# Optimization experiments

Hardware: AMD Instinct MI355X
Metric: run time of the kernel (lower is better)

## Reference

```python
import jax, jax.numpy as jnp
import numpy as np

# dims: L=seq_len, B=batch, D=n_d (hidden), PROJ=n_proj, H=heads, DEPTH=layers, V=vocab
L, B, D, PROJ, H, DEPTH, V = 1024, 4, 1024, 256, 8, 4, 32000
HD = PROJ // H          # head dim = 32
NEG = -10000.0          # additive causal mask value used by Model.set_mask


def setup_inputs() -> dict:
    key = jax.random.key(0)
    ks = jax.random.split(key, 12)
    s = (3.0 / D) ** 0.5  # init used by Model.init_weights (layer_norm-style)
    return {
        "x": jax.random.randint(ks[0], (L, B), 0, V),
        "y": jax.random.randint(ks[1], (L, B), 0, V),
        "hidden": jnp.zeros((DEPTH, B, D), jnp.float32),            # init_hidden
        "emb_W": jax.random.uniform(ks[2], (V, D), jnp.float32, -s, s),
        # SRU++ attention transform per layer: q-proj, kv-proj, output to 3*D (U matrices)
        "W1": jax.random.normal(ks[3], (DEPTH, D, PROJ), jnp.float32) / np.float32(np.sqrt(D)),
        "W2": jax.random.normal(ks[4], (DEPTH, PROJ, 2 * PROJ), jnp.float32) / np.float32(np.sqrt(PROJ)),
        "W3": jax.random.normal(ks[5], (DEPTH, PROJ, 3 * D), jnp.float32) / np.float32(np.sqrt(PROJ)),
        "alpha": jax.random.normal(ks[6], (DEPTH,), jnp.float32) * 0.1,  # rezero scalar (nonzero so attn path is live)
        "weight_c": jax.random.normal(ks[7], (DEPTH, 2 * D), jnp.float32) * 0.1,  # (v_f, v_r)
        # bias = (b_f, b_r); forget bias initialized to highway_bias = -3
        "bias": jnp.concatenate([jnp.full((DEPTH, D), -3.0, jnp.float32), jnp.zeros((DEPTH, D), jnp.float32)], axis=-1),
        "Wout": jax.random.uniform(ks[8], (D, V), jnp.float32, -s, s),
        "bout": jnp.zeros((V,), jnp.float32),
    }


def _attention_transform(h, W1, W2, W3, alpha, mask):
    # SRUppAttention (no memory, no layer_norm, dropout=0)
    z = jnp.einsum('lbd,dp->lbp', h, W1)                 # (L,B,PROJ) query / residual
    kv = jnp.einsum('lbp,pq->lbq', z, W2)                # (L,B,2*PROJ)
    k, v = jnp.split(kv, 2, axis=-1)
    q = z.reshape(L, B, H, HD) * (HD ** -0.5)
    k = k.reshape(L, B, H, HD)
    v = v.reshape(L, B, H, HD)
    scores = jnp.einsum('lbhd,sbhd->bhls', q, k) + mask  # causal additive mask
    attn = jax.nn.softmax(scores, axis=-1)
    out = jnp.einsum('bhls,sbhd->lbhd', attn, v).reshape(L, B, PROJ)
    out = out * alpha + z                                # rezero residual
    return jnp.einsum('lbp,pk->lbk', out, W3)            # U: (L,B,3*D)


def _sru_recurrence(U, residual, c0, vf, vr, bf, br):
    # SRU elementwise highway recurrence (k=3, identity activation, no rescale)
    u = U.reshape(L, B, D, 3)
    u0 = u[..., 0]
    u1 = u[..., 1] + bf
    u2 = u[..., 2] + br

    def step(c, xs):
        u0t, u1t, u2t, rt = xs                           # each (B,D)
        f = jax.nn.sigmoid(u1t + vf * c)
        c = f * c + (1.0 - f) * u0t
        r = jax.nn.sigmoid(u2t + vr * c)
        h = r * c + (1.0 - r) * rt                       # highway on layer input
        return c, h

    c_last, hs = jax.lax.scan(step, c0, (u0, u1, u2, residual))
    return hs, c_last


def reference(x, y, hidden, emb_W, W1, W2, W3, alpha, weight_c, bias, Wout, bout):
    mask = jnp.triu(jnp.full((L, L), NEG, jnp.float32), 1)   # Model.set_mask, mem_len=0
    h = emb_W[x]                                             # (L,B,D) embedding lookup
    for i in range(DEPTH):
        U = _attention_transform(h, W1[i], W2[i], W3[i], alpha[i], mask)
        h, _ = _sru_recurrence(U, h, hidden[i],
                               weight_c[i, :D], weight_c[i, D:],
                               bias[i, :D], bias[i, D:])
    logits = jnp.einsum('lbd,dv->lbv', h, Wout) + bout       # (L,B,V)
    logp = jax.nn.log_softmax(logits, axis=-1)
    loss = -jnp.take_along_axis(logp, y[..., None], axis=-1)[..., 0]  # (L,B) per-token CE
    return loss
```

## Files before the change

### kernel.cpp

```cpp
#include <hip/hip_runtime.h>
#include <hip/hip_bf16.h>
#include <stdint.h>

#define L_ 1024
#define B_ 4
#define D_ 1024
#define PROJ_ 256
#define H_ 8
#define V_ 32000
#define M_ 4096

typedef __bf16 bf16x8 __attribute__((ext_vector_type(8)));
typedef float f32x4 __attribute__((ext_vector_type(4)));

#define AS3(p) ((__attribute__((address_space(3))) void*)(p))
#define AS1(p) ((const __attribute__((address_space(1))) void*)(p))

__global__ __launch_bounds__(256) void k_embed(const int* __restrict__ x,
                                               const float* __restrict__ emb,
                                               __hip_bfloat16* __restrict__ h) {
  int gid = blockIdx.x * 256 + threadIdx.x;
  int row = gid >> 8;
  int d0 = (gid & 255) << 2;
  int tok = x[row];
  const float4 v = *(const float4*)(emb + (size_t)tok * D_ + d0);
  union { __hip_bfloat16 o[4]; uint2 u; } cv;
  cv.o[0] = __float2bfloat16(v.x);
  cv.o[1] = __float2bfloat16(v.y);
  cv.o[2] = __float2bfloat16(v.z);
  cv.o[3] = __float2bfloat16(v.w);
  *(uint2*)(h + (size_t)row * D_ + d0) = cv.u;
}

__global__ __launch_bounds__(256) void k_transpose(const float* __restrict__ in,
                                                   __hip_bfloat16* __restrict__ out,
                                                   int K, int N,
                                                   long in_stride, long out_stride) {
  __shared__ float t[64][65];
  in += (size_t)blockIdx.z * in_stride;
  out += (size_t)blockIdx.z * out_stride;
  int n0 = blockIdx.x * 64, k0 = blockIdx.y * 64;
  int r = threadIdx.x >> 4, c4 = (threadIdx.x & 15) << 2;
#pragma unroll
  for (int p = 0; p < 4; p++) {
    float4 v = *(const float4*)(in + (size_t)(k0 + p * 16 + r) * N + n0 + c4);
    t[p * 16 + r][c4 + 0] = v.x;
    t[p * 16 + r][c4 + 1] = v.y;
    t[p * 16 + r][c4 + 2] = v.z;
    t[p * 16 + r][c4 + 3] = v.w;
  }
  __syncthreads();
  int n = threadIdx.x >> 2, kg = (threadIdx.x & 3) << 4;
  union { __hip_bfloat16 b[16]; uint4 u[2]; } cv;
#pragma unroll
  for (int i = 0; i < 16; i++) cv.b[i] = __float2bfloat16(t[kg + i][n]);
  uint4* op = (uint4*)(out + (size_t)(n0 + n) * K + k0 + kg);
  op[0] = cv.u[0];
  op[1] = cv.u[1];
}

template <bool CLS>
__global__ __launch_bounds__(256) void k_gemm_bt(
    const __hip_bfloat16* __restrict__ A, const __hip_bfloat16* __restrict__ Bt,
    __hip_bfloat16* __restrict__ C, int K, int N,
    const float* __restrict__ bout, const int* __restrict__ y,
    float2* __restrict__ lse, float* __restrict__ logitY) {
  __shared__ __hip_bfloat16 As[128 * 64];
  __shared__ __hip_bfloat16 Bs[128 * 64];
  const int tid = threadIdx.x;
  const int lane = tid & 63, wave = tid >> 6;
  const int quad = lane >> 4, l16 = lane & 15;
  const int wm = wave & 1, wn = wave >> 1;
  const int row0 = blockIdx.x * 128, col0 = blockIdx.y * 128;

  f32x4 acc[4][4] = {};

  const __hip_bfloat16* Abase = A + (size_t)row0 * K;
  const __hip_bfloat16* Bbase = Bt + (size_t)col0 * K;
  const int m_s = tid >> 3;
  const int ko_sw = (((tid & 7) ^ (m_s & 7)) << 3);
  const int xr = l16 & 7;

  for (int k0 = 0; k0 < K; k0 += 64) {
    __syncthreads();
#pragma unroll
    for (int call = 0; call < 4; call++) {
      int m = m_s + call * 32;
      __builtin_amdgcn_global_load_lds(AS1(Abase + (size_t)m * K + k0 + ko_sw),
                                       AS3(As + (call * 256 + wave * 64) * 8),
                                       16, 0, 0);
      __builtin_amdgcn_global_load_lds(AS1(Bbase + (size_t)m * K + k0 + ko_sw),
                                       AS3(Bs + (call * 256 + wave * 64) * 8),
                                       16, 0, 0);
    }
    __syncthreads();
#pragma unroll
    for (int kk = 0; kk < 2; kk++) {
      bf16x8 af[4], bfr[4];
#pragma unroll
      for (int mi = 0; mi < 4; mi++)
        af[mi] = *(const bf16x8*)(As + (wm * 64 + mi * 16 + l16) * 64 +
                                  (((kk * 4 + quad) ^ xr) << 3));
#pragma unroll
      for (int ni = 0; ni < 4; ni++)
        bfr[ni] = *(const bf16x8*)(Bs + (wn * 64 + ni * 16 + l16) * 64 +
                                   (((kk * 4 + quad) ^ xr) << 3));
#pragma unroll
      for (int mi = 0; mi < 4; mi++)
#pragma unroll
        for (int ni = 0; ni < 4; ni++)
          acc[mi][ni] = __builtin_amdgcn_mfma_f32_16x16x32_bf16(af[mi], bfr[ni],
                                                                acc[mi][ni], 0, 0, 0);
    }
  }

  if constexpr (!CLS) {
#pragma unroll
    for (int mi = 0; mi < 4; mi++)
#pragma unroll
      for (int ni = 0; ni < 4; ni++)
#pragma unroll
        for (int r = 0; r < 4; r++) {
          int row = row0 + wm * 64 + mi * 16 + quad * 4 + r;
          int col = col0 + wn * 64 + ni * 16 + l16;
          C[(size_t)row * N + col] = __float2bfloat16(acc[mi][ni][r]);
        }
  } else {
    const int chunk = blockIdx.y * 2 + wn;
    float bv[4];
#pragma unroll
    for (int ni = 0; ni < 4; ni++)
      bv[ni] = bout[col0 + wn * 64 + ni * 16 + l16];
#pragma unroll
    for (int mi = 0; mi < 4; mi++) {
#pragma unroll
      for (int r = 0; r < 4; r++) {
        int row = row0 + wm * 64 + mi * 16 + quad * 4 + r;
        float v0 = acc[mi][0][r] + bv[0];
        float v1 = acc[mi][1][r] + bv[1];
        float v2 = acc[mi][2][r] + bv[2];
        float v3 = acc[mi][3][r] + bv[3];
        int yv = y[row];
        int cb = col0 + wn * 64 + l16;
        if (yv == cb + 0)  logitY[row] = v0;
        if (yv == cb + 16) logitY[row] = v1;
        if (yv == cb + 32) logitY[row] = v2;
        if (yv == cb + 48) logitY[row] = v3;
        float m = fmaxf(fmaxf(v0, v1), fmaxf(v2, v3));
#pragma unroll
        for (int off = 1; off < 16; off <<= 1)
          m = fmaxf(m, __shfl_xor(m, off, 64));
        float s = __expf(v0 - m) + __expf(v1 - m) + __expf(v2 - m) + __expf(v3 - m);
#pragma unroll
        for (int off = 1; off < 16; off <<= 1)
          s += __shfl_xor(s, off, 64);
        if (l16 == 0)
          lse[(size_t)chunk * M_ + row] = make_float2(m, s);
      }
    }
  }
}

__global__ __launch_bounds__(512, 2) void k_gemm_cls256(
    const __hip_bfloat16* __restrict__ A, const __hip_bfloat16* __restrict__ Bt,
    int K, const float* __restrict__ bout, const int* __restrict__ y,
    float2* __restrict__ lse, float* __restrict__ logitY) {
  __shared__ __align__(16) __hip_bfloat16 As[2][16384];
  __shared__ __align__(16) __hip_bfloat16 Bs[2][16384];
  const int tid = threadIdx.x;
  const int lane = tid & 63, wave = tid >> 6;
  const int quad = lane >> 4, l16 = lane & 15;
  const int wm = wave >> 2, wn = wave & 3;

  const int bid = blockIdx.y * 16 + blockIdx.x;
  const int swzb = (bid & 7) * 250 + (bid >> 3);
  const int bx = swzb & 15, by = swzb >> 4;
  const int row0 = bx * 256, col0 = by * 256;

  const int m_l = wave * 8 + (lane >> 3);
  const int sw = ((lane & 7) ^ (lane >> 3)) << 3;
  const __hip_bfloat16* Ag = A + (size_t)(row0 + m_l) * K + sw;
  const __hip_bfloat16* Bg = Bt + (size_t)(col0 + m_l) * K + sw;

#define STAGE_A(buf, r, ko)                                                   \
  __builtin_amdgcn_global_load_lds(AS1(Ag + (size_t)(r) * 64 * K + (ko)),     \
                                   AS3(&As[buf][((r) * 64 + wave * 8) * 64]), \
                                   16, 0, 0)
#define STAGE_B(buf, r, ko)                                                   \
  __builtin_amdgcn_global_load_lds(AS1(Bg + (size_t)(r) * 64 * K + (ko)),     \
                                   AS3(&Bs[buf][((r) * 64 + wave * 8) * 64]), \
                                   16, 0, 0)

  const int aoff = (wm * 128 + l16) * 64;
  const int boff = (wn * 64 + l16) * 64;
  const int cc0 = ((quad) ^ (l16 & 7)) << 3;
  const int cc1 = ((4 + quad) ^ (l16 & 7)) << 3;

  f32x4 acc[8][4] = {};
  bf16x8 a4[4], b0[4], b1[4];

#define DS_B(buf, breg, cck)                                                  \
  do {                                                                        \
    _Pragma("unroll") for (int ni = 0; ni < 4; ++ni)                          \
        breg[ni] = *(const bf16x8*)(&Bs[buf][boff + ni * 1024 + (cck)]);      \
  } while (0)

#define DS_A(buf, mlo, cck)                                                   \
  do {                                                                        \
    _Pragma("unroll") for (int mi = 0; mi < 4; ++mi)                          \
        a4[mi] = *(const bf16x8*)(&As[buf][aoff + ((mlo) + mi) * 1024 + (cck)]); \
  } while (0)

#define MFMA_Q(mlo, breg)                                                     \
  do {                                                                        \
    __builtin_amdgcn_s_barrier();                                             \
    asm volatile("s_waitcnt lgkmcnt(0)" ::: "memory");                        \
    __builtin_amdgcn_sched_barrier(0);                                        \
    __builtin_amdgcn_s_setprio(1);                                            \
    _Pragma("unroll") for (int mi = 0; mi < 4; ++mi)                          \
        _Pragma("unroll") for (int ni = 0; ni < 4; ++ni)                      \
            acc[(mlo) + mi][ni] = __builtin_amdgcn_mfma_f32_16x16x32_bf16(    \
                a4[mi], breg[ni], acc[(mlo) + mi][ni], 0, 0, 0);              \
    __builtin_amdgcn_s_setprio(0);                                            \
  } while (0)

#define BAR() __builtin_amdgcn_s_barrier()

  STAGE_A(0, 0, 0); STAGE_A(0, 1, 0); STAGE_A(0, 2, 0); STAGE_A(0, 3, 0);
  STAGE_B(0, 0, 0); STAGE_B(0, 1, 0); STAGE_B(0, 2, 0); STAGE_B(0, 3, 0);
  STAGE_B(1, 0, 64); STAGE_B(1, 1, 64); STAGE_B(1, 2, 64); STAGE_B(1, 3, 64);
  asm volatile("s_waitcnt vmcnt(4)" ::: "memory");
  BAR();

  for (int i = 0; i < 7; ++i) {
    const size_t kT1 = (size_t)i * 128 + 64;
    const size_t kN0 = (size_t)i * 128 + 128;
    const size_t kN1 = (size_t)i * 128 + 192;
    DS_B(0, b0, cc0); DS_A(0, 0, cc0);
    STAGE_A(1, 0, kT1); STAGE_A(1, 1, kT1); STAGE_A(1, 2, kT1); STAGE_A(1, 3, kT1);
    MFMA_Q(0, b0); BAR();
    DS_B(0, b1, cc1); DS_A(0, 0, cc1);
    MFMA_Q(0, b1); BAR();
    DS_A(0, 4, cc0);
    STAGE_B(0, 0, kN0); STAGE_B(0, 1, kN0);
    MFMA_Q(4, b0); BAR();
    DS_A(0, 4, cc1);
    STAGE_B(0, 2, kN0); STAGE_B(0, 3, kN0);
    MFMA_Q(4, b1);
    asm volatile("s_waitcnt vmcnt(4)" ::: "memory");
    BAR();
    DS_B(1, b0, cc0); DS_A(1, 0, cc0);
    STAGE_A(0, 0, kN0); STAGE_A(0, 1, kN0); STAGE_A(0, 2, kN0); STAGE_A(0, 3, kN0);
    MFMA_Q(0, b0); BAR();
    DS_B(1, b1, cc1); DS_A(1, 0, cc1);
    MFMA_Q(0, b1); BAR();
    DS_A(1, 4, cc0);
    STAGE_B(1, 0, kN1); STAGE_B(1, 1, kN1);
    MFMA_Q(4, b0); BAR();
    DS_A(1, 4, cc1);
    STAGE_B(1, 2, kN1); STAGE_B(1, 3, kN1);
    MFMA_Q(4, b1);
    asm volatile("s_waitcnt vmcnt(4)" ::: "memory");
    BAR();
  }
  {
    const size_t kT1 = (size_t)7 * 128 + 64;
    DS_B(0, b0, cc0); DS_A(0, 0, cc0);
    STAGE_A(1, 0, kT1); STAGE_A(1, 1, kT1); STAGE_A(1, 2, kT1); STAGE_A(1, 3, kT1);
    MFMA_Q(0, b0); BAR();
    DS_B(0, b1, cc1); DS_A(0, 0, cc1);
    MFMA_Q(0, b1); BAR();
    DS_A(0, 4, cc0);
    MFMA_Q(4, b0); BAR();
    DS_A(0, 4, cc1);
    MFMA_Q(4, b1);
    asm volatile("s_waitcnt vmcnt(0)" ::: "memory");
    BAR();
    DS_B(1, b0, cc0); DS_A(1, 0, cc0);
    MFMA_Q(0, b0); BAR();
    DS_B(1, b1, cc1); DS_A(1, 0, cc1);
    MFMA_Q(0, b1); BAR();
    DS_A(1, 4, cc0);
    MFMA_Q(4, b0); BAR();
    DS_A(1, 4, cc1);
    MFMA_Q(4, b1);
  }

  const int chunk = by * 4 + wn;
  float bv[4];
#pragma unroll
  for (int ni = 0; ni < 4; ++ni)
    bv[ni] = bout[col0 + wn * 64 + ni * 16 + l16];
#pragma unroll
  for (int mi = 0; mi < 8; ++mi) {
#pragma unroll
    for (int r = 0; r < 4; ++r) {
      int row = row0 + wm * 128 + mi * 16 + quad * 4 + r;
      float v0 = acc[mi][0][r] + bv[0];
      float v1 = acc[mi][1][r] + bv[1];
      float v2 = acc[mi][2][r] + bv[2];
      float v3 = acc[mi][3][r] + bv[3];
      int yv = y[row];
      int cb = col0 + wn * 64 + l16;
      if (yv == cb + 0)  logitY[row] = v0;
      if (yv == cb + 16) logitY[row] = v1;
      if (yv == cb + 32) logitY[row] = v2;
      if (yv == cb + 48) logitY[row] = v3;
      float m = fmaxf(fmaxf(v0, v1), fmaxf(v2, v3));
#pragma unroll
      for (int off = 1; off < 16; off <<= 1)
        m = fmaxf(m, __shfl_xor(m, off, 64));
      float s = __expf(v0 - m) + __expf(v1 - m) + __expf(v2 - m) + __expf(v3 - m);
#pragma unroll
      for (int off = 1; off < 16; off <<= 1)
        s += __shfl_xor(s, off, 64);
      if (l16 == 0)
        lse[(size_t)chunk * M_ + row] = make_float2(m, s);
    }
  }
#undef STAGE_A
#undef STAGE_B
#undef DS_A
#undef DS_B
#undef MFMA_Q
#undef BAR
}

__global__ __launch_bounds__(256) void k_gemm_cls_f32(
    const __hip_bfloat16* __restrict__ A, const float* __restrict__ B,
    int K, int N, const float* __restrict__ bout, const int* __restrict__ y,
    float2* __restrict__ lse, float* __restrict__ logitY) {
  __shared__ __hip_bfloat16 As[128 * 40];
  __shared__ __hip_bfloat16 Bs[128 * 40];
  const int tid = threadIdx.x;
  const int lane = tid & 63, wave = tid >> 6;
  const int quad = lane >> 4, l16 = lane & 15;
  const int wm = wave & 1, wn = wave >> 1;
  const int row0 = blockIdx.x * 128, col0 = blockIdx.y * 128;
  f32x4 acc[4][4] = {};
  const int a_m = tid >> 1, a_k = (tid & 1) << 4;
  const int b_k = tid >> 3, b_n = (tid & 7) << 4;
  for (int k0 = 0; k0 < K; k0 += 32) {
    const uint4* ap = (const uint4*)(A + (size_t)(row0 + a_m) * K + k0 + a_k);
    uint4 av0 = ap[0];
    uint4 av1 = ap[1];
    const float* bp = B + (size_t)(k0 + b_k) * N + col0 + b_n;
    float4 bv0 = *(const float4*)(bp + 0);
    float4 bv1 = *(const float4*)(bp + 4);
    float4 bv2 = *(const float4*)(bp + 8);
    float4 bv3 = *(const float4*)(bp + 12);
    __syncthreads();
    *(uint4*)(As + a_m * 40 + a_k) = av0;
    *(uint4*)(As + a_m * 40 + a_k + 8) = av1;
    {
      float tmp[16] = {bv0.x, bv0.y, bv0.z, bv0.w, bv1.x, bv1.y, bv1.z, bv1.w,
                       bv2.x, bv2.y, bv2.z, bv2.w, bv3.x, bv3.y, bv3.z, bv3.w};
#pragma unroll
      for (int j = 0; j < 16; j++)
        Bs[(b_n + j) * 40 + b_k] = __float2bfloat16(tmp[j]);
    }
    __syncthreads();
    bf16x8 af[4], bfr[4];
#pragma unroll
    for (int mi = 0; mi < 4; mi++)
      af[mi] = *(const bf16x8*)(As + (wm * 64 + mi * 16 + l16) * 40 + quad * 8);
#pragma unroll
    for (int ni = 0; ni < 4; ni++)
      bfr[ni] = *(const bf16x8*)(Bs + (wn * 64 + ni * 16 + l16) * 40 + quad * 8);
#pragma unroll
    for (int mi = 0; mi < 4; mi++)
#pragma unroll
      for (int ni = 0; ni < 4; ni++)
        acc[mi][ni] = __builtin_amdgcn_mfma_f32_16x16x32_bf16(af[mi], bfr[ni],
                                                              acc[mi][ni], 0, 0, 0);
  }
  const int chunk = blockIdx.y * 2 + wn;
  float bv[4];
#pragma unroll
  for (int ni = 0; ni < 4; ni++)
    bv[ni] = bout[col0 + wn * 64 + ni * 16 + l16];
#pragma unroll
  for (int mi = 0; mi < 4; mi++) {
#pragma unroll
    for (int r = 0; r < 4; r++) {
      int row = row0 + wm * 64 + mi * 16 + quad * 4 + r;
      float v0 = acc[mi][0][r] + bv[0];
      float v1 = acc[mi][1][r] + bv[1];
      float v2 = acc[mi][2][r] + bv[2];
      float v3 = acc[mi][3][r] + bv[3];
      int yv = y[row];
      int cb = col0 + wn * 64 + l16;
      if (yv == cb + 0)  logitY[row] = v0;
      if (yv == cb + 16) logitY[row] = v1;
      if (yv == cb + 32) logitY[row] = v2;
      if (yv == cb + 48) logitY[row] = v3;
      float m = fmaxf(fmaxf(v0, v1), fmaxf(v2, v3));
#pragma unroll
      for (int off = 1; off < 16; off <<= 1)
        m = fmaxf(m, __shfl_xor(m, off, 64));
      float s = __expf(v0 - m) + __expf(v1 - m) + __expf(v2 - m) + __expf(v3 - m);
#pragma unroll
      for (int off = 1; off < 16; off <<= 1)
        s += __shfl_xor(s, off, 64);
      if (l16 == 0)
        lse[(size_t)chunk * M_ + row] = make_float2(m, s);
    }
  }
}

__global__ __launch_bounds__(256) void k_attn_mfma(
    const __hip_bfloat16* __restrict__ z, const __hip_bfloat16* __restrict__ kv,
    __hip_bfloat16* __restrict__ ao, const float* __restrict__ alpha_p) {
  __shared__ __hip_bfloat16 Qs[64 * 40];
  __shared__ __hip_bfloat16 Ks[128 * 40];
  __shared__ __hip_bfloat16 Vt[32 * 136];
  __shared__ __hip_bfloat16 Ps[64 * 136];
  const int tid = threadIdx.x;
  const int lane = tid & 63, wave = tid >> 6;
  const int quad = lane >> 4, l16 = lane & 15;
  const int bh = blockIdx.y, b = bh >> 3, h = bh & 7;
  const int q0 = blockIdx.x * 64;
  const float scale = 0.17677669529663687f;

  {
    int r = tid >> 2, c = (tid & 3) << 3;
    *(uint4*)(Qs + r * 40 + c) =
        *(const uint4*)(z + ((size_t)(q0 + r) * B_ + b) * PROJ_ + h * 32 + c);
  }

  float m_i[4] = {-1e30f, -1e30f, -1e30f, -1e30f};
  float l_i[4] = {0.f, 0.f, 0.f, 0.f};
  f32x4 o_acc[2] = {};

  const int ntile = (q0 + 191) >> 7;

  for (int t = 0; t < ntile; t++) {
    const int s0 = t << 7;
    __syncthreads();
    {
      int r = tid >> 1, c = (tid & 1) << 4;
      const uint4* kp =
          (const uint4*)(kv + ((size_t)(s0 + r) * B_ + b) * 512 + h * 32 + c);
      *(uint4*)(Ks + r * 40 + c) = kp[0];
      *(uint4*)(Ks + r * 40 + c + 8) = kp[1];
    }
    {
      int s = tid >> 1, dbase = (tid & 1) << 4;
      const __hip_bfloat16* vp =
          kv + ((size_t)(s0 + s) * B_ + b) * 512 + 256 + h * 32 + dbase;
      union { uint4 u; __hip_bfloat16 e[8]; } t0, t1;
      t0.u = *(const uint4*)vp;
      t1.u = *(const uint4*)(vp + 8);
#pragma unroll
      for (int j = 0; j < 8; j++) {
        Vt[(dbase + j) * 136 + s] = t0.e[j];
        Vt[(dbase + 8 + j) * 136 + s] = t1.e[j];
      }
    }
    __syncthreads();

    f32x4 sacc[8] = {};
    {
      bf16x8 aq = *(const bf16x8*)(Qs + (wave * 16 + l16) * 40 + quad * 8);
#pragma unroll
      for (int ni = 0; ni < 8; ni++) {
        bf16x8 bk = *(const bf16x8*)(Ks + (ni * 16 + l16) * 40 + quad * 8);
        sacc[ni] = __builtin_amdgcn_mfma_f32_16x16x32_bf16(aq, bk, sacc[ni], 0, 0, 0);
      }
    }

#pragma unroll
    for (int r = 0; r < 4; r++) {
      const int qrow = q0 + wave * 16 + quad * 4 + r;
      float mx = -1e30f;
#pragma unroll
      for (int ni = 0; ni < 8; ni++) {
        int s = s0 + ni * 16 + l16;
        float v = (s <= qrow) ? sacc[ni][r] * scale : -1e30f;
        sacc[ni][r] = v;
        mx = fmaxf(mx, v);
      }
#pragma unroll
      for (int off = 1; off < 16; off <<= 1)
        mx = fmaxf(mx, __shfl_xor(mx, off, 64));
      float mnew = fmaxf(m_i[r], mx);
      float al = __expf(m_i[r] - mnew);
      m_i[r] = mnew;
      float ps = 0.f;
#pragma unroll
      for (int ni = 0; ni < 8; ni++) {
        float p = __expf(sacc[ni][r] - mnew);
        Ps[(wave * 16 + quad * 4 + r) * 136 + ni * 16 + l16] = __float2bfloat16(p);
        ps += p;
      }
#pragma unroll
      for (int off = 1; off < 16; off <<= 1)
        ps += __shfl_xor(ps, off, 64);
      l_i[r] = l_i[r] * al + ps;
      o_acc[0][r] *= al;
      o_acc[1][r] *= al;
    }

#pragma unroll
    for (int ks = 0; ks < 4; ks++) {
      bf16x8 ap = *(const bf16x8*)(Ps + (wave * 16 + l16) * 136 + ks * 32 + quad * 8);
#pragma unroll
      for (int ni = 0; ni < 2; ni++) {
        bf16x8 bv = *(const bf16x8*)(Vt + (ni * 16 + l16) * 136 + ks * 32 + quad * 8);
        o_acc[ni] = __builtin_amdgcn_mfma_f32_16x16x32_bf16(ap, bv, o_acc[ni], 0, 0, 0);
      }
    }
  }

  const float arz = alpha_p[0];
#pragma unroll
  for (int ni = 0; ni < 2; ni++)
#pragma unroll
    for (int r = 0; r < 4; r++) {
      int row = q0 + wave * 16 + quad * 4 + r;
      size_t oi = ((size_t)row * B_ + b) * PROJ_ + h * 32 + ni * 16 + l16;
      float res = __bfloat162float(z[oi]);
      ao[oi] = __float2bfloat16(o_acc[ni][r] / l_i[r] * arz + res);
    }
}

__global__ __launch_bounds__(64) void k_sru(const __hip_bfloat16* __restrict__ U,
                                            __hip_bfloat16* __restrict__ h,
                                            const float* __restrict__ hidden,
                                            const float* __restrict__ wc,
                                            const float* __restrict__ bias) {
  int tid = blockIdx.x * 64 + threadIdx.x;
  int b = tid >> 10, d = tid & 1023;
  float vf = wc[d], vr = wc[D_ + d];
  float bfs = bias[d], brs = bias[D_ + d];
  float c = hidden[b * D_ + d];
  const __hip_bfloat16* up = U + (size_t)b * 3 * D_ + 3 * d;
  __hip_bfloat16* hp = h + (size_t)b * D_ + d;
  const int US = B_ * 3 * D_, HS = B_ * D_;
  for (int l0 = 0; l0 < L_; l0 += 8) {
    float u0[8], u1[8], u2[8], rs[8];
#pragma unroll
    for (int j = 0; j < 8; j++) {
      u0[j] = __bfloat162float(up[(size_t)j * US + 0]);
      u1[j] = __bfloat162float(up[(size_t)j * US + 1]);
      u2[j] = __bfloat162float(up[(size_t)j * US + 2]);
      rs[j] = __bfloat162float(hp[(size_t)j * HS]);
    }
#pragma unroll
    for (int j = 0; j < 8; j++) {
      float f = __builtin_amdgcn_rcpf(1.f + __expf(-(u1[j] + bfs + vf * c)));
      c = u0[j] + f * (c - u0[j]);
      float r = __builtin_amdgcn_rcpf(1.f + __expf(-(u2[j] + brs + vr * c)));
      hp[(size_t)j * HS] = __float2bfloat16(rs[j] + r * (c - rs[j]));
    }
    up += (size_t)8 * US;
    hp += (size_t)8 * HS;
  }
}

__global__ __launch_bounds__(256) void k_finalize(const float2* __restrict__ lse,
                                                  const float* __restrict__ logitY,
                                                  float* __restrict__ out) {
  int row = blockIdx.x * 256 + threadIdx.x;
  float M = -1e30f, S = 0.f;
  for (int c = 0; c < V_ / 64; c++) {
    float2 p = lse[(size_t)c * M_ + row];
    if (p.x > M) {
      S = S * __expf(M - p.x) + p.y;
      M = p.x;
    } else {
      S += p.y * __expf(p.x - M);
    }
  }
  out[row] = M + logf(S) - logitY[row];
}

extern "C" void kernel_launch(void* const* d_in, const int* in_sizes, int n_in,
                              void* d_out, int out_size, void* d_ws, size_t ws_size,
                              hipStream_t stream) {
  const int* x = (const int*)d_in[0];
  const int* y = (const int*)d_in[1];
  const float* hidden = (const float*)d_in[2];
  const float* emb = (const float*)d_in[3];
  const float* W1 = (const float*)d_in[4];
  const float* W2 = (const float*)d_in[5];
  const float* W3 = (const float*)d_in[6];
  const float* alpha = (const float*)d_in[7];
  const float* wc = (const float*)d_in[8];
  const float* bias = (const float*)d_in[9];
  const float* Wout = (const float*)d_in[10];
  const float* bout = (const float*)d_in[11];

  char* ws = (char*)d_ws;
  __hip_bfloat16* h16  = (__hip_bfloat16*)(ws + 0);
  __hip_bfloat16* z16  = (__hip_bfloat16*)(ws + 8388608);
  __hip_bfloat16* kv16 = (__hip_bfloat16*)(ws + 10485760);
  __hip_bfloat16* ao16 = (__hip_bfloat16*)(ws + 14680064);
  __hip_bfloat16* W1t  = (__hip_bfloat16*)(ws + 16777216);
  __hip_bfloat16* W2t  = (__hip_bfloat16*)(ws + 18874368);
  __hip_bfloat16* W3t  = (__hip_bfloat16*)(ws + 19922944);
  __hip_bfloat16* U16  = (__hip_bfloat16*)(ws + 26214400);
  const bool fast = ws_size >= 109723648ull;
  __hip_bfloat16* Woutt = (__hip_bfloat16*)(ws + 26214400);
  float2* lse    = (float2*)(ws + (fast ? 93323264u : 26214400u));
  float* logitY  = (float*)(ws + (fast ? 109707264u : 42598400u));
  float* out     = (float*)d_out;

  k_embed<<<4096, 256, 0, stream>>>(x, emb, h16);
  k_transpose<<<dim3(4, 16, 4), 256, 0, stream>>>(W1, W1t, D_, PROJ_,
                                                  (long)D_ * PROJ_, (long)PROJ_ * D_);
  k_transpose<<<dim3(8, 4, 4), 256, 0, stream>>>(W2, W2t, PROJ_, 2 * PROJ_,
                                                 (long)PROJ_ * 2 * PROJ_,
                                                 (long)2 * PROJ_ * PROJ_);
  k_transpose<<<dim3(48, 4, 4), 256, 0, stream>>>(W3, W3t, PROJ_, 3 * D_,
                                                  (long)PROJ_ * 3 * D_,
                                                  (long)3 * D_ * PROJ_);
  for (int i = 0; i < 4; i++) {
    k_gemm_bt<false><<<dim3(32, 2), 256, 0, stream>>>(
        h16, W1t + (size_t)i * PROJ_ * D_, z16, D_, PROJ_,
        nullptr, nullptr, nullptr, nullptr);
    k_gemm_bt<false><<<dim3(32, 4), 256, 0, stream>>>(
        z16, W2t + (size_t)i * 2 * PROJ_ * PROJ_, kv16, PROJ_, 2 * PROJ_,
        nullptr, nullptr, nullptr, nullptr);
    k_attn_mfma<<<dim3(16, 32), 256, 0, stream>>>(z16, kv16, ao16, alpha + i);
    k_gemm_bt<false><<<dim3(32, 24), 256, 0, stream>>>(
        ao16, W3t + (size_t)i * 3 * D_ * PROJ_, U16, PROJ_, 3 * D_,
        nullptr, nullptr, nullptr, nullptr);
    k_sru<<<64, 64, 0, stream>>>(U16, h16, hidden + (size_t)i * B_ * D_,
                                 wc + (size_t)i * 2 * D_, bias + (size_t)i * 2 * D_);
  }
  if (fast) {
    k_transpose<<<dim3(500, 16, 1), 256, 0, stream>>>(Wout, Woutt, D_, V_, 0, 0);
    k_gemm_cls256<<<dim3(16, 125), 512, 0, stream>>>(h16, Woutt, D_, bout, y,
                                                     lse, logitY);
  } else {
    k_gemm_cls_f32<<<dim3(32, V_ / 128), 256, 0, stream>>>(
        h16, Wout, D_, V_, bout, y, lse, logitY);
  }
  k_finalize<<<16, 256, 0, stream>>>(lse, logitY, out);
}
```

Measured before the change: 1.444 ms.

## Permute W3 columns for coalesced SRU loads and double-buffer the SRU recurrence

The W3 transpose now writes its output rows in a permuted order, so the U matrix is stored as three contiguous D-wide planes (u0, u1, u2) rather than interleaved triples. Each SRU thread therefore reads adjacent addresses across the wavefront, giving coalesced accesses. The SRU loop also double-buffers its loads, prefetching the next 8 timesteps while the current 8 are computed, to hide memory latency in the serial recurrence. The cost is more registers per thread and an extra modulo/divide in the transpose kernel.

```diff
diff --git a/kernel.cpp b/kernel.cpp
--- a/kernel.cpp
+++ b/kernel.cpp
@@ -35,7 +35,8 @@
 __global__ __launch_bounds__(256) void k_transpose(const float* __restrict__ in,
                                                    __hip_bfloat16* __restrict__ out,
                                                    int K, int N,
-                                                   long in_stride, long out_stride) {
+                                                   long in_stride, long out_stride,
+                                                   int perm3) {
   __shared__ float t[64][65];
   in += (size_t)blockIdx.z * in_stride;
   out += (size_t)blockIdx.z * out_stride;
@@ -54,7 +55,9 @@
   union { __hip_bfloat16 b[16]; uint4 u[2]; } cv;
 #pragma unroll
   for (int i = 0; i < 16; i++) cv.b[i] = __float2bfloat16(t[kg + i][n]);
-  uint4* op = (uint4*)(out + (size_t)(n0 + n) * K + k0 + kg);
+  int nn = n0 + n;
+  if (perm3) nn = (nn % 3) * D_ + nn / 3;
+  uint4* op = (uint4*)(out + (size_t)nn * K + k0 + kg);
   op[0] = cv.u[0];
   op[1] = cv.u[1];
 }
@@ -534,28 +537,43 @@
   float vf = wc[d], vr = wc[D_ + d];
   float bfs = bias[d], brs = bias[D_ + d];
   float c = hidden[b * D_ + d];
-  const __hip_bfloat16* up = U + (size_t)b * 3 * D_ + 3 * d;
+  const int US = B_ * 3 * D_, HS = B_ * D_;
+  const __hip_bfloat16* up = U + (size_t)b * 3 * D_ + d;
   __hip_bfloat16* hp = h + (size_t)b * D_ + d;
-  const int US = B_ * 3 * D_, HS = B_ * D_;
-  for (int l0 = 0; l0 < L_; l0 += 8) {
-    float u0[8], u1[8], u2[8], rs[8];
-#pragma unroll
-    for (int j = 0; j < 8; j++) {
-      u0[j] = __bfloat162float(up[(size_t)j * US + 0]);
-      u1[j] = __bfloat162float(up[(size_t)j * US + 1]);
-      u2[j] = __bfloat162float(up[(size_t)j * US + 2]);
-      rs[j] = __bfloat162float(hp[(size_t)j * HS]);
-    }
-#pragma unroll
-    for (int j = 0; j < 8; j++) {
-      float f = __builtin_amdgcn_rcpf(1.f + __expf(-(u1[j] + bfs + vf * c)));
-      c = u0[j] + f * (c - u0[j]);
-      float r = __builtin_amdgcn_rcpf(1.f + __expf(-(u2[j] + brs + vr * c)));
-      hp[(size_t)j * HS] = __float2bfloat16(rs[j] + r * (c - rs[j]));
-    }
-    up += (size_t)8 * US;
-    hp += (size_t)8 * HS;
-  }
+
+#define SRU_LOAD(u0a, u1a, u2a, rsa, base_l)                                  \
+  do {                                                                        \
+    _Pragma("unroll") for (int j = 0; j < 8; j++) {                           \
+      size_t o = (size_t)((base_l) + j) * US;                                 \
+      u0a[j] = __bfloat162float(up[o]);                                       \
+      u1a[j] = __bfloat162float(up[o + D_]);                                  \
+      u2a[j] = __bfloat162float(up[o + 2 * D_]);                              \
+      rsa[j] = __bfloat162float(hp[(size_t)((base_l) + j) * HS]);             \
+    }                                                                         \
+  } while (0)
+
+#define SRU_COMP(u0a, u1a, u2a, rsa, base_l)                                  \
+  do {                                                                        \
+    _Pragma("unroll") for (int j = 0; j < 8; j++) {                           \
+      float f = __builtin_amdgcn_rcpf(1.f + __expf(-(u1a[j] + bfs + vf * c)));\
+      c = u0a[j] + f * (c - u0a[j]);                                          \
+      float r = __builtin_amdgcn_rcpf(1.f + __expf(-(u2a[j] + brs + vr * c)));\
+      hp[(size_t)((base_l) + j) * HS] =                                       \
+          __float2bfloat16(rsa[j] + r * (c - rsa[j]));                        \
+    }                                                                         \
+  } while (0)
+
+  float a0[8], a1[8], a2[8], ar[8];
+  float c0[8], c1[8], c2[8], cr[8];
+  SRU_LOAD(a0, a1, a2, ar, 0);
+  for (int l0 = 0; l0 < L_; l0 += 16) {
+    SRU_LOAD(c0, c1, c2, cr, l0 + 8);
+    SRU_COMP(a0, a1, a2, ar, l0);
+    if (l0 + 16 < L_) SRU_LOAD(a0, a1, a2, ar, l0 + 16);
+    SRU_COMP(c0, c1, c2, cr, l0 + 8);
+  }
+#undef SRU_LOAD
+#undef SRU_COMP
 }
 
 __global__ __launch_bounds__(256) void k_finalize(const float2* __restrict__ lse,
@@ -608,13 +626,13 @@
 
   k_embed<<<4096, 256, 0, stream>>>(x, emb, h16);
   k_transpose<<<dim3(4, 16, 4), 256, 0, stream>>>(W1, W1t, D_, PROJ_,
-                                                  (long)D_ * PROJ_, (long)PROJ_ * D_);
+                                                  (long)D_ * PROJ_, (long)PROJ_ * D_, 0);
   k_transpose<<<dim3(8, 4, 4), 256, 0, stream>>>(W2, W2t, PROJ_, 2 * PROJ_,
                                                  (long)PROJ_ * 2 * PROJ_,
-                                                 (long)2 * PROJ_ * PROJ_);
+                                                 (long)2 * PROJ_ * PROJ_, 0);
   k_transpose<<<dim3(48, 4, 4), 256, 0, stream>>>(W3, W3t, PROJ_, 3 * D_,
                                                   (long)PROJ_ * 3 * D_,
-                                                  (long)3 * D_ * PROJ_);
+                                                  (long)3 * D_ * PROJ_, 1);
   for (int i = 0; i < 4; i++) {
     k_gemm_bt<false><<<dim3(32, 2), 256, 0, stream>>>(
         h16, W1t + (size_t)i * PROJ_ * D_, z16, D_, PROJ_,
@@ -630,7 +648,7 @@
                                  wc + (size_t)i * 2 * D_, bias + (size_t)i * 2 * D_);
   }
   if (fast) {
-    k_transpose<<<dim3(500, 16, 1), 256, 0, stream>>>(Wout, Woutt, D_, V_, 0, 0);
+    k_transpose<<<dim3(500, 16, 1), 256, 0, stream>>>(Wout, Woutt, D_, V_, 0, 0, 0);
     k_gemm_cls256<<<dim3(16, 125), 512, 0, stream>>>(h16, Woutt, D_, bout, y,
                                                      lse, logitY);
   } else {
```

After: 1.496 ms. +3.6%, slower.
